# Performance work log

Hardware: AMD Instinct MI355X
Metric: run time of the kernel (lower is better)

## Reference

```python
import jax, jax.numpy as jnp
import numpy as np

GRID_SIZE = 5
SPLINE_ORDER = 3


def _haar_filters():
    # db1 (Haar) decomposition filters, matching wavelet.create_wavelet_filter:
    # dec_lo[::-1] = [s, s], dec_hi[::-1] = [s, -s]; rec filters are identical for Haar.
    s = np.float32(1.0 / np.sqrt(2.0))
    lo = np.array([s, s], np.float32)
    hi = np.array([s, -s], np.float32)
    # f = a.unsqueeze(0) * b.unsqueeze(1)  ->  f[p, q] = a[q] * b[p]
    def outer(a, b):
        return b[:, None] * a[None, :]
    dec = np.stack([outer(lo, lo), outer(lo, hi), outer(hi, lo), outer(hi, hi)], 0)  # (4,2,2): LL,LH,HL,HH
    return jnp.asarray(dec), jnp.asarray(dec)


def depthwise_conv5(x, w, b):
    # torch Conv2d(C, C, 5, padding='same', groups=C)
    y = jax.lax.conv_general_dilated(
        x, w, window_strides=(1, 1), padding=[(2, 2), (2, 2)],
        dimension_numbers=('NCHW', 'OIHW', 'NCHW'), feature_group_count=x.shape[1])
    return y + b[None, :, None, None]


def kan_linear(x, base_w, spline_w, scaler):
    # efficient-kan KANLinear: base SiLU linear + B-spline linear over last dim.
    in_f = x.shape[-1]
    out_f = base_w.shape[0]
    shp = x.shape
    xf = x.reshape(-1, in_f)                      # (N, in)
    h = 2.0 / GRID_SIZE                           # grid_range [-1, 1]
    grid_1d = jnp.arange(-SPLINE_ORDER, GRID_SIZE + SPLINE_ORDER + 1, dtype=xf.dtype) * h - 1.0
    grid = jnp.broadcast_to(grid_1d, (in_f, grid_1d.shape[0]))  # (in, G+2k+1)
    xe = xf[:, :, None]
    bases = ((xe >= grid[:, :-1]) & (xe < grid[:, 1:])).astype(xf.dtype)
    for k in range(1, SPLINE_ORDER + 1):
        bases = ((xe - grid[:, :-(k + 1)]) / (grid[:, k:-1] - grid[:, :-(k + 1)]) * bases[..., :-1]
                 + (grid[:, k + 1:] - xe) / (grid[:, k + 1:] - grid[:, 1:-k]) * bases[..., 1:])
    # bases: (N, in, G+k)
    base_out = jax.nn.silu(xf) @ base_w.T
    sw = spline_w * scaler[:, :, None]            # scaled_spline_weight (out, in, G+k)
    spline_out = jnp.einsum('nig,oig->no', bases, sw)
    return (base_out + spline_out).reshape(*shp[:-1], out_f)


def setup_inputs() -> dict:
    key = jax.random.key(0)
    ks = jax.random.split(key, 6)
    C, H, W, B = 32, 256, 256, 4
    in_f = C * 4  # 128
    return {
        'x': jax.random.normal(ks[0], (B, C, H, W), jnp.float32),
        'conv_w': jax.random.normal(ks[1], (C, 1, 5, 5), jnp.float32) * 0.2,
        'conv_b': jax.random.normal(ks[2], (C,), jnp.float32) * 0.02,
        'kan_base_w': jax.random.normal(ks[3], (in_f, in_f), jnp.float32) * (1.0 / np.sqrt(in_f)),
        'kan_spline_w': jax.random.normal(ks[4], (in_f, in_f, GRID_SIZE + SPLINE_ORDER), jnp.float32) * 0.1,
        'kan_spline_scaler': 1.0 + 0.1 * jax.random.normal(ks[5], (in_f, in_f), jnp.float32),
    }


def reference(x, conv_w, conv_b, kan_base_w, kan_spline_w, kan_spline_scaler):
    dec, rec = _haar_filters()
    b, c, hh, ww = x.shape
    # Level-1 skip: depthwise base_conv on full-res input
    skip = depthwise_conv5(x, conv_w, conv_b)
    # Haar wavelet transform (stride-2 non-overlapping 2x2 depthwise conv) via reshape+einsum
    x5 = x.reshape(b, c, hh // 2, 2, ww // 2, 2)
    wt = jnp.einsum('bcipjq,kpq->bckij', x5, dec)  # (b, c, 4, h/2, w/2)
    # Subband KAN over last (width) dim of 128 == in_channels*4 -> msi_kan branch
    z = kan_linear(wt, kan_base_w, kan_spline_w, kan_spline_scaler)
    # Inverse wavelet (stride-2 conv_transpose) via einsum scatter
    y = jnp.einsum('bckij,kpq->bcipjq', z, rec).reshape(b, c, hh, ww)
    return y + skip
```

## Files before the change

### kernel.cpp

```cpp
#include <hip/hip_runtime.h>
#include <hip/hip_bf16.h>

using f32x4 = __attribute__((ext_vector_type(4))) float;
using s16x8 = __attribute__((ext_vector_type(8))) short;
using u32x4 = __attribute__((ext_vector_type(4))) unsigned;

constexpr int Bn = 4, Cc = 32, Hh = 256, Ww = 256;
constexpr int H2 = 128, W2 = 128;
constexpr int NF = 128;
constexpr int KTOT = 1152;

__device__ __forceinline__ short f2bf(float f) {
    union { float f; unsigned u; } v; v.f = f;
    unsigned r = v.u + 0x7fffu + ((v.u >> 16) & 1u);
    return (short)(r >> 16);
}

__device__ __forceinline__ unsigned pk_bf16(float a, float b) {
    union { __hip_bfloat162 h; unsigned u; } c;
    c.h.x = __float2bfloat16(a);
    c.h.y = __float2bfloat16(b);
    return c.u;
}

__device__ __forceinline__ void gload_lds16(const void* g, void* l) {
    __builtin_amdgcn_global_load_lds(
        (const __attribute__((address_space(1))) unsigned*)g,
        (__attribute__((address_space(3))) unsigned*)l, 16, 0, 0);
}

__device__ __forceinline__ void window128(float wD, float wC, float wB, float wA,
                                          int ci, unsigned W[4]) {
    unsigned long long P = ((unsigned long long)pk_bf16(wB, wA) << 32)
                         | (unsigned long long)pk_bf16(wD, wC);
    int sh = ci * 16 - 48;
    unsigned long long sl = P << (sh & 63);
    unsigned long long sr = P >> ((-sh) & 63);
    unsigned long long lo = (sh < 0) ? sr : ((sh < 64) ? sl : 0ull);
    int shh = sh - 64;
    unsigned long long sl2 = P << (shh & 63);
    unsigned long long sr2 = P >> ((-shh) & 63);
    unsigned long long hi = (shh >= 0) ? sl2 : (((-shh) < 64) ? sr2 : 0ull);
    W[0] = (unsigned)lo; W[1] = (unsigned)(lo >> 32);
    W[2] = (unsigned)hi; W[3] = (unsigned)(hi >> 32);
}

__global__ __launch_bounds__(256) void k_wbuild(const float* __restrict__ base_w,
                                                const float* __restrict__ spline_w,
                                                const float* __restrict__ scaler,
                                                short* __restrict__ Bg) {
    int idx = blockIdx.x * 256 + threadIdx.x;
    int tile = idx >> 9;
    int r = idx & 511;
    int lane = r >> 3, q = r & 7;
    int ni = tile / 36; int rem = tile - ni * 36;
    int jg = rem / 9;   int ks = rem - jg * 9;
    int o = ni * 16 + (lane & 15);
    int kk = ks * 32 + (lane >> 4) * 8 + q;
    int g = kk >> 5, jl = kk & 31;
    int j = jg * 32 + jl;
    float v = (g == 0) ? base_w[o * NF + j]
                       : spline_w[(long)(o * NF + j) * 8 + (g - 1)] * scaler[o * NF + j];
    Bg[idx] = f2bf(v);
}

__device__ __forceinline__ void ldrow6(const float* xrp, int j, bool rok, float o[6]) {
    float2 lo = (rok && j >= 1)   ? *(const float2*)(xrp + 2 * j - 2) : make_float2(0.f, 0.f);
    float2 mi = rok               ? *(const float2*)(xrp + 2 * j)     : make_float2(0.f, 0.f);
    float2 hi = (rok && j <= 126) ? *(const float2*)(xrp + 2 * j + 2) : make_float2(0.f, 0.f);
    o[0] = lo.x; o[1] = lo.y; o[2] = mi.x; o[3] = mi.y; o[4] = hi.x; o[5] = hi.y;
}

__global__ __launch_bounds__(256, 2) void k_fused(const float* __restrict__ x,
                                                  const float* __restrict__ cw,
                                                  const float* __restrict__ cb,
                                                  float* __restrict__ out,
                                                  const short* __restrict__ Bg) {
    __shared__ __align__(16) short Bsh[72 * 512];
    const int t = threadIdx.x;
    const int lane = t & 63;
    const int w = t >> 6;
    const int blk = blockIdx.x;
    const int plane = blk >> 2;
    const int band = blk & 3;
    const int i0 = band << 5;
    const int jg0 = blk & 3;
    const int il = lane & 15;
    const int fg = lane >> 4;

    const float sB = (w & 2) ? -1.f : 1.f;
    const float sC = (w & 1) ? -1.f : 1.f;
    const float sD = sB * sC;

    const float* xbase = x + (long)plane * Hh * Ww;
    const float* xr0a = xbase + (long)(2 * (i0 + il)) * Ww;
    const float* xr1a = xr0a + Ww;
    const float* xr0b = xbase + (long)(2 * (i0 + il + 16)) * Ww;
    const float* xr1b = xr0b + Ww;

    f32x4 acc[2][8];
#pragma unroll
    for (int mi = 0; mi < 2; ++mi)
#pragma unroll
        for (int ni = 0; ni < 8; ++ni)
            acc[mi][ni] = (f32x4){0.f, 0.f, 0.f, 0.f};

    for (int j = 0; j < 4; ++j) {
        const int jg = (jg0 + j) & 3;
        const int cb2 = jg * 64 + fg * 16;

#pragma unroll
        for (int s = 0; s < 18; ++s) {
            int q = s * 4 + w;
            int ni = q / 9, ks = q - ni * 9;
            gload_lds16(&Bg[(long)(((ni * 4 + jg) * 9 + ks) << 9) + lane * 8],
                        &Bsh[q << 9]);
        }

        u32x4 afr[2][9];
#pragma unroll
        for (int mi = 0; mi < 2; ++mi) {
            const float* r0 = mi ? xr0b : xr0a;
            const float* r1 = mi ? xr1b : xr1a;
#pragma unroll
            for (int p = 0; p < 4; ++p) {
                f32x4 va = *(const f32x4*)(r0 + cb2 + 4 * p);
                f32x4 vb = *(const f32x4*)(r1 + cb2 + 4 * p);
                float vv[2];
                vv[0] = 0.5f * (va[0] + sB * va[1] + sC * vb[0] + sD * vb[1]);
                vv[1] = 0.5f * (va[2] + sB * va[3] + sC * vb[2] + sD * vb[3]);
                float sl2[2]; unsigned Wf[2][4];
#pragma unroll
                for (int e = 0; e < 2; ++e) {
                    float v = vv[e];
                    float ex = __builtin_amdgcn_exp2f(-1.442695040888963f * v);
                    sl2[e] = v * __builtin_amdgcn_rcpf(1.0f + ex);
                    float xs = __builtin_fmaf(v, 2.5f, 5.5f);
                    xs = fminf(fmaxf(xs, 0.0f), 10.999f);
                    float cf = floorf(xs);
                    float u = xs - cf;
                    int ci = (int)cf;
                    float u2 = u * u, u3 = u2 * u;
                    float wA = u3 * (1.f / 6.f);
                    float wB = (1.f + 3.f * u + 3.f * u2 - 3.f * u3) * (1.f / 6.f);
                    float wC = (4.f - 6.f * u2 + 3.f * u3) * (1.f / 6.f);
                    float um = 1.f - u;
                    float wD = um * um * um * (1.f / 6.f);
                    window128(wD, wC, wB, wA, ci, Wf[e]);
                }
                afr[mi][0][p] = pk_bf16(sl2[0], sl2[1]);
#pragma unroll
                for (int g = 1; g <= 8; ++g) {
                    int wq = (g - 1) >> 1;
                    unsigned sel = ((g - 1) & 1) ? 0x07060302u : 0x05040100u;
                    afr[mi][g][p] = __builtin_amdgcn_perm(Wf[1][wq], Wf[0][wq], sel);
                }
            }
        }

        __syncthreads();

#pragma unroll
        for (int ks = 0; ks < 9; ++ks) {
            s16x8 bfr[8];
#pragma unroll
            for (int ni = 0; ni < 8; ++ni)
                bfr[ni] = *(const s16x8*)&Bsh[((ni * 9 + ks) << 9) + lane * 8];
#pragma unroll
            for (int mi = 0; mi < 2; ++mi) {
                s16x8 a = __builtin_bit_cast(s16x8, afr[mi][ks]);
#pragma unroll
                for (int ni = 0; ni < 8; ++ni)
                    acc[mi][ni] = __builtin_amdgcn_mfma_f32_16x16x32_bf16(
                        a, bfr[ni], acc[mi][ni], 0, 0, 0);
            }
        }
        __syncthreads();
    }

    constexpr int ZP = 132;
    float* zsh = (float*)Bsh;
#pragma unroll
    for (int mi = 0; mi < 2; ++mi)
#pragma unroll
        for (int rr = 0; rr < 4; ++rr)
#pragma unroll
            for (int ni = 0; ni < 8; ++ni)
                zsh[(w * 32 + mi * 16 + fg * 4 + rr) * ZP + ni * 16 + il]
                    = acc[mi][ni][rr];
    __syncthreads();

    const int c = plane & 31;
    float cwr[25];
#pragma unroll
    for (int q = 0; q < 25; ++q) cwr[q] = cw[c * 25 + q];
    const float bias = cb[c];
    float* outp = out + (long)plane * Hh * Ww;
    const int qyg = t >> 6;

#pragma unroll
    for (int qxh = 0; qxh < 2; ++qxh) {
        const int jq = qxh * 64 + lane;
        float xv[6][6];
#pragma unroll
        for (int a = 0; a < 8; ++a) {
            const int ql = qyg * 8 + a;
            const int orow = 2 * (i0 + ql);
            if (a == 0) {
#pragma unroll
                for (int r6 = 0; r6 < 6; ++r6) {
                    int xr = orow - 2 + r6;
                    ldrow6(xbase + (long)xr * Ww, jq, xr >= 0 && xr < Hh, xv[r6]);
                }
            } else {
#pragma unroll
                for (int r6 = 0; r6 < 4; ++r6)
#pragma unroll
                    for (int c6 = 0; c6 < 6; ++c6) xv[r6][c6] = xv[r6 + 2][c6];
#pragma unroll
                for (int r6 = 4; r6 < 6; ++r6) {
                    int xr = orow - 2 + r6;
                    ldrow6(xbase + (long)xr * Ww, jq, xr >= 0 && xr < Hh, xv[r6]);
                }
            }
            float z0 = zsh[(ql) * ZP + jq];
            float z1 = zsh[(32 + ql) * ZP + jq];
            float z2 = zsh[(64 + ql) * ZP + jq];
            float z3 = zsh[(96 + ql) * ZP + jq];
            float y00 = 0.5f * (z0 + z1 + z2 + z3);
            float y01 = 0.5f * (z0 + z1 - z2 - z3);
            float y10 = 0.5f * (z0 - z1 + z2 - z3);
            float y11 = 0.5f * (z0 - z1 - z2 + z3);
            float s00 = bias, s01 = bias, s10 = bias, s11 = bias;
#pragma unroll
            for (int ky = 0; ky < 5; ++ky)
#pragma unroll
                for (int kx = 0; kx < 5; ++kx) {
                    float wv = cwr[ky * 5 + kx];
                    s00 += wv * xv[ky][kx];
                    s01 += wv * xv[ky][kx + 1];
                    s10 += wv * xv[ky + 1][kx];
                    s11 += wv * xv[ky + 1][kx + 1];
                }
            float* op = outp + (long)orow * Ww + 2 * jq;
            *(float2*)op        = make_float2(s00 + y00, s01 + y01);
            *(float2*)(op + Ww) = make_float2(s10 + y10, s11 + y11);
        }
    }
}

extern "C" void kernel_launch(void* const* d_in, const int* in_sizes, int n_in,
                              void* d_out, int out_size, void* d_ws, size_t ws_size,
                              hipStream_t stream) {
    const float* x        = (const float*)d_in[0];
    const float* conv_w   = (const float*)d_in[1];
    const float* conv_b   = (const float*)d_in[2];
    const float* base_w   = (const float*)d_in[3];
    const float* spline_w = (const float*)d_in[4];
    const float* scaler   = (const float*)d_in[5];
    float* out = (float*)d_out;
    short* Bg  = (short*)d_ws;

    k_wbuild<<<(NF * KTOT) / 256, 256, 0, stream>>>(base_w, spline_w, scaler, Bg);
    k_fused<<<512, 256, 0, stream>>>(x, conv_w, conv_b, out, Bg);
}
```

Before: 56.39 us.

## Interleave depthwise conv skip computation into MFMA loop iterations

Moves the 5x5 depthwise conv skip path into the per-jg loop so each wave computes two output row-pairs per iteration, right after its MFMA block. The aim is to overlap the VALU- and memory-heavy convolution with the matrix work and spread the epilogue load. Boundary handling switches to clamped addresses with multiplicative masks, and s_setprio is raised around the MFMA section. In exchange, the epilogue now reads the partial output back from global memory and adds the wavelet term, which costs an extra read-modify-write pass over the output. The vertical row reuse in the convolution is also reduced, since rows are reloaded for each pair.

```diff
diff --git a/kernel.cpp b/kernel.cpp
--- a/kernel.cpp
+++ b/kernel.cpp
@@ -64,13 +64,6 @@
     Bg[idx] = f2bf(v);
 }
 
-__device__ __forceinline__ void ldrow6(const float* xrp, int j, bool rok, float o[6]) {
-    float2 lo = (rok && j >= 1)   ? *(const float2*)(xrp + 2 * j - 2) : make_float2(0.f, 0.f);
-    float2 mi = rok               ? *(const float2*)(xrp + 2 * j)     : make_float2(0.f, 0.f);
-    float2 hi = (rok && j <= 126) ? *(const float2*)(xrp + 2 * j + 2) : make_float2(0.f, 0.f);
-    o[0] = lo.x; o[1] = lo.y; o[2] = mi.x; o[3] = mi.y; o[4] = hi.x; o[5] = hi.y;
-}
-
 __global__ __launch_bounds__(256, 2) void k_fused(const float* __restrict__ x,
                                                   const float* __restrict__ cw,
                                                   const float* __restrict__ cb,
@@ -98,6 +91,14 @@
     const float* xr0b = xbase + (long)(2 * (i0 + il + 16)) * Ww;
     const float* xr1b = xr0b + Ww;
 
+    const int c = plane & 31;
+    float cwr[25];
+#pragma unroll
+    for (int q = 0; q < 25; ++q) cwr[q] = cw[c * 25 + q];
+    const float bias = cb[c];
+    float* outp = out + (long)plane * Hh * Ww;
+    const int qyg = w;
+
     f32x4 acc[2][8];
 #pragma unroll
     for (int mi = 0; mi < 2; ++mi)
@@ -160,6 +161,7 @@
 
         __syncthreads();
 
+        __builtin_amdgcn_s_setprio(1);
 #pragma unroll
         for (int ks = 0; ks < 9; ++ks) {
             s16x8 bfr[8];
@@ -175,6 +177,60 @@
                         a, bfr[ni], acc[mi][ni], 0, 0, 0);
             }
         }
+        __builtin_amdgcn_s_setprio(0);
+
+#pragma unroll
+        for (int qxh = 0; qxh < 2; ++qxh) {
+            const int jq = qxh * 64 + lane;
+            const float mlo = (jq >= 1) ? 1.f : 0.f;
+            const float mhi = (jq <= 126) ? 1.f : 0.f;
+            const int clo = (jq >= 1) ? (2 * jq - 2) : 0;
+            const int cmid = 2 * jq;
+            const int chi = (jq <= 126) ? (2 * jq + 2) : 252;
+            float xv[6][6];
+#pragma unroll
+            for (int aa = 0; aa < 2; ++aa) {
+                const int ql = qyg * 8 + 2 * j + aa;
+                const int orow = 2 * (i0 + ql);
+                const int rlo = (aa == 0) ? 0 : 4;
+                if (aa) {
+#pragma unroll
+                    for (int r6 = 0; r6 < 4; ++r6)
+#pragma unroll
+                        for (int c6 = 0; c6 < 6; ++c6) xv[r6][c6] = xv[r6 + 2][c6];
+                }
+#pragma unroll
+                for (int r6 = 0; r6 < 6; ++r6) {
+                    if (r6 < rlo) continue;
+                    int xr = orow - 2 + r6;
+                    int xrc = min(max(xr, 0), Hh - 1);
+                    float mrow = (xr >= 0 && xr < Hh) ? 1.f : 0.f;
+                    const float* xrp = xbase + (long)xrc * Ww;
+                    float2 lo = *(const float2*)(xrp + clo);
+                    float2 mi2 = *(const float2*)(xrp + cmid);
+                    float2 hi = *(const float2*)(xrp + chi);
+                    float ml = mlo * mrow, mh = mhi * mrow;
+                    xv[r6][0] = lo.x * ml;    xv[r6][1] = lo.y * ml;
+                    xv[r6][2] = mi2.x * mrow; xv[r6][3] = mi2.y * mrow;
+                    xv[r6][4] = hi.x * mh;    xv[r6][5] = hi.y * mh;
+                }
+                float s00 = bias, s01 = bias, s10 = bias, s11 = bias;
+#pragma unroll
+                for (int ky = 0; ky < 5; ++ky)
+#pragma unroll
+                    for (int kx = 0; kx < 5; ++kx) {
+                        float wv = cwr[ky * 5 + kx];
+                        s00 += wv * xv[ky][kx];
+                        s01 += wv * xv[ky][kx + 1];
+                        s10 += wv * xv[ky + 1][kx];
+                        s11 += wv * xv[ky + 1][kx + 1];
+                    }
+                float* op = outp + (long)orow * Ww + 2 * jq;
+                *(float2*)op        = make_float2(s00, s01);
+                *(float2*)(op + Ww) = make_float2(s10, s11);
+            }
+        }
+
         __syncthreads();
     }
 
@@ -190,39 +246,13 @@
                     = acc[mi][ni][rr];
     __syncthreads();
 
-    const int c = plane & 31;
-    float cwr[25];
-#pragma unroll
-    for (int q = 0; q < 25; ++q) cwr[q] = cw[c * 25 + q];
-    const float bias = cb[c];
-    float* outp = out + (long)plane * Hh * Ww;
-    const int qyg = t >> 6;
-
 #pragma unroll
     for (int qxh = 0; qxh < 2; ++qxh) {
         const int jq = qxh * 64 + lane;
-        float xv[6][6];
 #pragma unroll
         for (int a = 0; a < 8; ++a) {
             const int ql = qyg * 8 + a;
             const int orow = 2 * (i0 + ql);
-            if (a == 0) {
-#pragma unroll
-                for (int r6 = 0; r6 < 6; ++r6) {
-                    int xr = orow - 2 + r6;
-                    ldrow6(xbase + (long)xr * Ww, jq, xr >= 0 && xr < Hh, xv[r6]);
-                }
-            } else {
-#pragma unroll
-                for (int r6 = 0; r6 < 4; ++r6)
-#pragma unroll
-                    for (int c6 = 0; c6 < 6; ++c6) xv[r6][c6] = xv[r6 + 2][c6];
-#pragma unroll
-                for (int r6 = 4; r6 < 6; ++r6) {
-                    int xr = orow - 2 + r6;
-                    ldrow6(xbase + (long)xr * Ww, jq, xr >= 0 && xr < Hh, xv[r6]);
-                }
-            }
             float z0 = zsh[(ql) * ZP + jq];
             float z1 = zsh[(32 + ql) * ZP + jq];
             float z2 = zsh[(64 + ql) * ZP + jq];
@@ -231,20 +261,13 @@
             float y01 = 0.5f * (z0 + z1 - z2 - z3);
             float y10 = 0.5f * (z0 - z1 + z2 - z3);
             float y11 = 0.5f * (z0 - z1 - z2 + z3);
-            float s00 = bias, s01 = bias, s10 = bias, s11 = bias;
-#pragma unroll
-            for (int ky = 0; ky < 5; ++ky)
-#pragma unroll
-                for (int kx = 0; kx < 5; ++kx) {
-                    float wv = cwr[ky * 5 + kx];
-                    s00 += wv * xv[ky][kx];
-                    s01 += wv * xv[ky][kx + 1];
-                    s10 += wv * xv[ky + 1][kx];
-                    s11 += wv * xv[ky + 1][kx + 1];
-                }
             float* op = outp + (long)orow * Ww + 2 * jq;
-            *(float2*)op        = make_float2(s00 + y00, s01 + y01);
-            *(float2*)(op + Ww) = make_float2(s10 + y10, s11 + y11);
+            float2 p0 = *(float2*)op;
+            float2 p1 = *(float2*)(op + Ww);
+            p0.x += y00; p0.y += y01;
+            p1.x += y10; p1.y += y11;
+            *(float2*)op        = p0;
+            *(float2*)(op + Ww) = p1;
         }
     }
 }
```

New measurement: 67.20 us. 19.2% more time.
